# Optimization experiments

Hardware: AMD Instinct MI355X
Metric: run time of the kernel (lower is better)

## Reference

```python
import jax, jax.numpy as jnp
import numpy as np
import math


def _attn(q, k, v):
    # q,k,v: [B, S, d] (d == 1 here). bmm -> scale -> softmax -> bmm.
    scale = 1.0 / math.sqrt(q.shape[2])
    e = jnp.einsum('bsd,btd->bst', q, k) * scale  # [B, S, S]
    w = jax.nn.softmax(e, axis=2)
    return jnp.einsum('bst,btd->bsd', w, v)


def setup_inputs() -> dict:
    key = jax.random.key(0)
    ks = jax.random.split(key, 12)
    B, D = 32, 768
    CLF_OUT = 7
    inp = {}
    names = ['sentence', 'target_spkr_snts', 'other_spkr_snts', 'scene_desc', 'scene_sent']
    for i, name in enumerate(names):
        inp[name] = jax.random.normal(ks[i], (B, D), dtype=jnp.float32)
    inp['W_shared'] = jax.random.normal(ks[5], (768, 512), dtype=jnp.float32) * 0.02
    inp['b_shared'] = jnp.zeros((512,), dtype=jnp.float32)
    inp['W1'] = jax.random.normal(ks[6], (3840, 256), dtype=jnp.float32) * 0.02
    inp['b1'] = jnp.zeros((256,), dtype=jnp.float32)
    inp['W2'] = jax.random.normal(ks[7], (256, CLF_OUT), dtype=jnp.float32) * 0.02
    inp['b2'] = jnp.zeros((CLF_OUT,), dtype=jnp.float32)
    return inp


def reference(sentence, target_spkr_snts, other_spkr_snts, scene_desc, scene_sent,
              W_shared, b_shared, W1, b1, W2, b2):
    B = sentence.shape[0]
    s = sentence[..., None]             # [B, 768, 1]
    sd = scene_desc[..., None]
    ts = target_spkr_snts[..., None]
    oth = other_spkr_snts[..., None]
    ss = scene_sent[..., None]

    speaker_context = _attn(oth, ts, ts)   # [B, 768, 1]
    scene_context = _attn(ss, ss, sd)      # [B, 768, 1]

    sentence_shared = sentence @ W_shared + b_shared                     # [B, 512]
    scene_context_shared = scene_context.reshape(B, -1) @ W_shared + b_shared
    speaker_context_shared = speaker_context.reshape(B, -1) @ W_shared + b_shared

    fused = jnp.concatenate([s, scene_context, speaker_context], axis=1)  # [B, 2304, 1]
    z = _attn(fused, fused, fused)                                        # [B, 2304, 1]

    final = jnp.concatenate([z.reshape(B, -1), sentence_shared,
                             scene_context_shared, speaker_context_shared], axis=1)  # [B, 3840]
    h = jax.nn.relu(final @ W1 + b1)   # dropout is identity in eval mode
    return jax.nn.sigmoid(h @ W2 + b2)  # [B, 7]
```

## Files before the change

### kernel.cpp

```cpp
#include <hip/hip_runtime.h>
#include <math.h>

#define LOG2E 1.44269504088896340736f
typedef float v2f __attribute__((ext_vector_type(2)));


__device__ __forceinline__ void proj_512(
    const float* __restrict__ xsrc,
    const float* __restrict__ Ws,
    const float* __restrict__ bs,
    float* __restrict__ dst,
    float* xb,
    float (*red)[512],
    int tid)
{
    if (tid < 512) { xb[tid] = xsrc[tid]; }
    if (tid >= 256) { xb[tid + 256] = xsrc[tid + 256]; }
    __syncthreads();

    const int g = tid >> 7;
    const int q = tid & 127;
    const float4* __restrict__ Wv = (const float4*)Ws;
    float ax = 0.f, ay = 0.f, az = 0.f, aw = 0.f;
    #pragma unroll 8
    for (int k = g; k < 768; k += 4) {
        const float xv = xb[k];
        const float4 w = Wv[k * 128 + q];
        ax += xv * w.x; ay += xv * w.y; az += xv * w.z; aw += xv * w.w;
    }
    red[g][q * 4 + 0] = ax;
    red[g][q * 4 + 1] = ay;
    red[g][q * 4 + 2] = az;
    red[g][q * 4 + 3] = aw;
    __syncthreads();

    if (tid < 512) {
        float s = bs[tid] + red[0][tid] + red[1][tid] + red[2][tid] + red[3][tid];
        dst[tid] = s;
    }
}

__global__ __launch_bounds__(512) void k1_small_attn_proj0(
    const float* __restrict__ sentence,
    const float* __restrict__ target,
    const float* __restrict__ other,
    const float* __restrict__ scene_desc,
    const float* __restrict__ scene_sent,
    const float* __restrict__ Ws,
    const float* __restrict__ bs,
    float* __restrict__ ctx,
    float* __restrict__ final_)
{
    const int b = blockIdx.x;
    const int y = blockIdx.y;
    const int tid = threadIdx.x;
    __shared__ float s0[768];
    __shared__ float s1[768];
    __shared__ float red[4][512];

    if (y < 24) {
        const int part = y / 12;
        const int rg = y - part * 12;
        const float* qp; const float* kp; const float* vp;
        if (part == 0) { qp = scene_sent + b * 768; kp = qp;               vp = scene_desc + b * 768; }
        else           { qp = other + b * 768;      kp = target + b * 768; vp = kp; }
        for (int i = tid; i < 768; i += 512) { s0[i] = kp[i]; s1[i] = vp[i]; }
        __syncthreads();

        const int r   = rg * 64 + (tid >> 3);
        const int sub = tid & 7;
        const float qL = qp[r] * LOG2E;
        const v2f qL2 = {qL, qL};
        const float4* __restrict__ kv = (const float4*)s0;
        const float4* __restrict__ vv = (const float4*)s1;
        v2f n01 = {0.f, 0.f}, n23 = {0.f, 0.f}, d01 = {0.f, 0.f}, d23 = {0.f, 0.f};
        #pragma unroll 4
        for (int i = 0; i < 24; ++i) {
            const int j = sub + 8 * i;
            const float4 k4 = kv[j];
            const float4 v4 = vv[j];
            const v2f ka = {k4.x, k4.y}, kb = {k4.z, k4.w};
            const v2f va = {v4.x, v4.y}, vbv = {v4.z, v4.w};
            const v2f xa = qL2 * ka, xb2 = qL2 * kb;
            const v2f ea = {__builtin_amdgcn_exp2f(xa.x), __builtin_amdgcn_exp2f(xa.y)};
            const v2f eb = {__builtin_amdgcn_exp2f(xb2.x), __builtin_amdgcn_exp2f(xb2.y)};
            n01 += ea * va;  d01 += ea;
            n23 += eb * vbv; d23 += eb;
        }
        float num = (n01.x + n01.y) + (n23.x + n23.y);
        float den = (d01.x + d01.y) + (d23.x + d23.y);
        num += __shfl_xor(num, 1, 64); num += __shfl_xor(num, 2, 64); num += __shfl_xor(num, 4, 64);
        den += __shfl_xor(den, 1, 64); den += __shfl_xor(den, 2, 64); den += __shfl_xor(den, 4, 64);
        if (sub == 0)
            ctx[b * 1536 + part * 768 + r] = num / den;
    } else {
        proj_512(sentence + b * 768, Ws, bs, final_ + b * 3840 + 2304, s0, red, tid);
    }
}

__global__ __launch_bounds__(512) void k2_fused_attn_proj12(
    const float* __restrict__ sentence,
    const float* __restrict__ ctx,
    const float* __restrict__ Ws,
    const float* __restrict__ bs,
    float* __restrict__ final_)
{
    const int b = blockIdx.x;
    const int y = blockIdx.y;
    const int tid = threadIdx.x;
    __shared__ float vb[2304];
    __shared__ float red[4][512];

    if (y < 36) {
        for (int i = tid; i < 2304; i += 512)
            vb[i] = (i < 768) ? sentence[b * 768 + i] : ctx[b * 1536 + (i - 768)];
        __syncthreads();

        const int r   = y * 64 + (tid >> 3);
        const int sub = tid & 7;
        const float qL = vb[r] * LOG2E;
        const v2f qL2 = {qL, qL};
        const float4* __restrict__ fv = (const float4*)vb;
        v2f n01 = {0.f, 0.f}, n23 = {0.f, 0.f}, d01 = {0.f, 0.f}, d23 = {0.f, 0.f};
        #pragma unroll 4
        for (int i = 0; i < 72; ++i) {
            const int j = sub + 8 * i;
            const float4 f4 = fv[j];
            const v2f fa = {f4.x, f4.y}, fb = {f4.z, f4.w};
            const v2f xa = qL2 * fa, xb2 = qL2 * fb;
            const v2f ea = {__builtin_amdgcn_exp2f(xa.x), __builtin_amdgcn_exp2f(xa.y)};
            const v2f eb = {__builtin_amdgcn_exp2f(xb2.x), __builtin_amdgcn_exp2f(xb2.y)};
            n01 += ea * fa; d01 += ea;
            n23 += eb * fb; d23 += eb;
        }
        float num = (n01.x + n01.y) + (n23.x + n23.y);
        float den = (d01.x + d01.y) + (d23.x + d23.y);
        num += __shfl_xor(num, 1, 64); num += __shfl_xor(num, 2, 64); num += __shfl_xor(num, 4, 64);
        den += __shfl_xor(den, 1, 64); den += __shfl_xor(den, 2, 64); den += __shfl_xor(den, 4, 64);
        if (sub == 0)
            final_[b * 3840 + r] = num / den;
    } else {
        const int p = y - 35;
        proj_512(ctx + b * 1536 + (p - 1) * 768, Ws, bs,
                 final_ + b * 3840 + 2304 + p * 512, vb, red, tid);
    }
}

__global__ __launch_bounds__(1024) void mlp_part_kernel(
    const float* __restrict__ final_,
    const float* __restrict__ W1,
    float* __restrict__ hpart)
{
    const int b = blockIdx.x;
    const int c = blockIdx.y;
    const int tid = threadIdx.x;
    const int base = c * 480;

    __shared__ float fb[480];
    __shared__ float red[16][256];
    if (tid < 480) fb[tid] = final_[b * 3840 + base + tid];
    __syncthreads();

    const int g = tid >> 6;
    const int q = tid & 63;
    const float4* __restrict__ Wv = (const float4*)W1;
    float ax = 0.f, ay = 0.f, az = 0.f, aw = 0.f;
    const int l0 = g * 30;
    #pragma unroll 5
    for (int kk = 0; kk < 30; ++kk) {
        const float xv = fb[l0 + kk];
        const float4 w = Wv[(base + l0 + kk) * 64 + q];
        ax += xv * w.x; ay += xv * w.y; az += xv * w.z; aw += xv * w.w;
    }
    red[g][q * 4 + 0] = ax;
    red[g][q * 4 + 1] = ay;
    red[g][q * 4 + 2] = az;
    red[g][q * 4 + 3] = aw;
    __syncthreads();

    if (tid < 256) {
        float s = 0.f;
        #pragma unroll
        for (int g2 = 0; g2 < 16; ++g2) s += red[g2][tid];
        hpart[(b * 8 + c) * 256 + tid] = s;
    }
}

__global__ __launch_bounds__(512) void mlp_tail_kernel(
    const float* __restrict__ hpart,
    const float* __restrict__ b1,
    const float* __restrict__ W2,
    const float* __restrict__ b2,
    float* __restrict__ out)
{
    const int b = blockIdx.x;
    const int tid = threadIdx.x;

    __shared__ float hb[256];
    if (tid < 256) {
        float s = b1[tid];
        #pragma unroll
        for (int c = 0; c < 8; ++c) s += hpart[(b * 8 + c) * 256 + tid];
        hb[tid] = fmaxf(s, 0.f);
    }
    __syncthreads();

    const int w = tid >> 6;
    const int lane = tid & 63;
    if (w < 7) {
        float a = 0.f;
        #pragma unroll
        for (int c = lane; c < 256; c += 64)
            a += hb[c] * W2[c * 7 + w];
        #pragma unroll
        for (int off = 32; off > 0; off >>= 1)
            a += __shfl_down(a, off, 64);
        if (lane == 0)
            out[b * 7 + w] = 1.f / (1.f + __expf(-(a + b2[w])));
    }
}

extern "C" void kernel_launch(void* const* d_in, const int* in_sizes, int n_in,
                              void* d_out, int out_size, void* d_ws, size_t ws_size,
                              hipStream_t stream) {
    const float* sentence   = (const float*)d_in[0];
    const float* target     = (const float*)d_in[1];
    const float* other      = (const float*)d_in[2];
    const float* scene_desc = (const float*)d_in[3];
    const float* scene_sent = (const float*)d_in[4];
    const float* Ws         = (const float*)d_in[5];
    const float* bs         = (const float*)d_in[6];
    const float* W1         = (const float*)d_in[7];
    const float* b1         = (const float*)d_in[8];
    const float* W2         = (const float*)d_in[9];
    const float* b2         = (const float*)d_in[10];
    float* out = (float*)d_out;

    float* ctx    = (float*)d_ws;
    float* final_ = ctx + 32 * 1536;
    float* hpart  = final_ + 32 * 3840;

    k1_small_attn_proj0<<<dim3(32, 25), 512, 0, stream>>>(sentence, target, other,
                                                          scene_desc, scene_sent,
                                                          Ws, bs, ctx, final_);
    k2_fused_attn_proj12<<<dim3(32, 38), 512, 0, stream>>>(sentence, ctx, Ws, bs, final_);
    mlp_part_kernel<<<dim3(32, 8), 1024, 0, stream>>>(final_, W1, hpart);
    mlp_tail_kernel<<<32, 512, 0, stream>>>(hpart, b1, W2, b2, out);
}
```

Measured before the change: 61.10 us.

## Register-block attention rows per thread and halve block size

The attention loops now give each thread 4 query rows that share every loaded key/value float4, with 16 lanes splitting the key dimension instead of 8. Blocks shrink from 512 to 256 threads, and the projection helper is reworked so each thread handles two k-phases and two output columns. This cuts LDS reads per exp and reduces block-level overhead, but it raises register pressure and lengthens each thread's serial work.

Measured after the change: 66.98 us. +9.6%, slower.

```diff
diff --git a/kernel.cpp b/kernel.cpp
--- a/kernel.cpp
+++ b/kernel.cpp
@@ -5,17 +5,16 @@
 typedef float v2f __attribute__((ext_vector_type(2)));
 
 
-__device__ __forceinline__ void proj_512(
+__device__ __forceinline__ void proj_256(
     const float* __restrict__ xsrc,
     const float* __restrict__ Ws,
     const float* __restrict__ bs,
     float* __restrict__ dst,
     float* xb,
-    float (*red)[512],
+    float* redf,
     int tid)
 {
-    if (tid < 512) { xb[tid] = xsrc[tid]; }
-    if (tid >= 256) { xb[tid + 256] = xsrc[tid + 256]; }
+    for (int i = tid; i < 768; i += 256) xb[i] = xsrc[i];
     __syncthreads();
 
     const int g = tid >> 7;
@@ -23,24 +22,70 @@
     const float4* __restrict__ Wv = (const float4*)Ws;
     float ax = 0.f, ay = 0.f, az = 0.f, aw = 0.f;
     #pragma unroll 8
-    for (int k = g; k < 768; k += 4) {
+    for (int k = g; k < 768; k += 2) {
         const float xv = xb[k];
         const float4 w = Wv[k * 128 + q];
         ax += xv * w.x; ay += xv * w.y; az += xv * w.z; aw += xv * w.w;
     }
-    red[g][q * 4 + 0] = ax;
-    red[g][q * 4 + 1] = ay;
-    red[g][q * 4 + 2] = az;
-    red[g][q * 4 + 3] = aw;
-    __syncthreads();
-
-    if (tid < 512) {
-        float s = bs[tid] + red[0][tid] + red[1][tid] + red[2][tid] + red[3][tid];
-        dst[tid] = s;
-    }
-}
-
-__global__ __launch_bounds__(512) void k1_small_attn_proj0(
+    redf[g * 512 + q * 4 + 0] = ax;
+    redf[g * 512 + q * 4 + 1] = ay;
+    redf[g * 512 + q * 4 + 2] = az;
+    redf[g * 512 + q * 4 + 3] = aw;
+    __syncthreads();
+
+    dst[tid]       = bs[tid]       + redf[tid]       + redf[512 + tid];
+    dst[tid + 256] = bs[tid + 256] + redf[tid + 256] + redf[512 + tid + 256];
+}
+
+__device__ __forceinline__ void attn_r4(
+    const float* __restrict__ qsrc,
+    const float4* __restrict__ kv,
+    const float4* __restrict__ vv,
+    int n4, int rbase, int tid,
+    float* __restrict__ outp)
+{
+    const int i0  = rbase + (tid >> 4);
+    const int sub = tid & 15;
+    v2f q2[4];
+    #pragma unroll
+    for (int m = 0; m < 4; ++m) {
+        const float qL = qsrc[i0 + 16 * m] * LOG2E;
+        q2[m] = (v2f){qL, qL};
+    }
+    v2f n0[4], n1[4], d0[4], d1[4];
+    #pragma unroll
+    for (int m = 0; m < 4; ++m) {
+        n0[m] = (v2f){0.f, 0.f}; n1[m] = (v2f){0.f, 0.f};
+        d0[m] = (v2f){0.f, 0.f}; d1[m] = (v2f){0.f, 0.f};
+    }
+    #pragma unroll 2
+    for (int j = sub; j < n4; j += 16) {
+        const float4 k4 = kv[j];
+        const float4 v4 = vv[j];
+        const v2f ka = {k4.x, k4.y}, kb = {k4.z, k4.w};
+        const v2f va = {v4.x, v4.y}, vb2 = {v4.z, v4.w};
+        #pragma unroll
+        for (int m = 0; m < 4; ++m) {
+            const v2f xa = q2[m] * ka, xb = q2[m] * kb;
+            const v2f ea = {__builtin_amdgcn_exp2f(xa.x), __builtin_amdgcn_exp2f(xa.y)};
+            const v2f eb = {__builtin_amdgcn_exp2f(xb.x), __builtin_amdgcn_exp2f(xb.y)};
+            n0[m] += ea * va;  d0[m] += ea;
+            n1[m] += eb * vb2; d1[m] += eb;
+        }
+    }
+    #pragma unroll
+    for (int m = 0; m < 4; ++m) {
+        float num = (n0[m].x + n0[m].y) + (n1[m].x + n1[m].y);
+        float den = (d0[m].x + d0[m].y) + (d1[m].x + d1[m].y);
+        num += __shfl_xor(num, 1, 64); num += __shfl_xor(num, 2, 64);
+        num += __shfl_xor(num, 4, 64); num += __shfl_xor(num, 8, 64);
+        den += __shfl_xor(den, 1, 64); den += __shfl_xor(den, 2, 64);
+        den += __shfl_xor(den, 4, 64); den += __shfl_xor(den, 8, 64);
+        if (sub == 0) outp[i0 + 16 * m] = num / den;
+    }
+}
+
+__global__ __launch_bounds__(256) void k1_small_attn_proj0(
     const float* __restrict__ sentence,
     const float* __restrict__ target,
     const float* __restrict__ other,
@@ -56,7 +101,7 @@
     const int tid = threadIdx.x;
     __shared__ float s0[768];
     __shared__ float s1[768];
-    __shared__ float red[4][512];
+    __shared__ float redf[1024];
 
     if (y < 24) {
         const int part = y / 12;
@@ -64,41 +109,16 @@
         const float* qp; const float* kp; const float* vp;
         if (part == 0) { qp = scene_sent + b * 768; kp = qp;               vp = scene_desc + b * 768; }
         else           { qp = other + b * 768;      kp = target + b * 768; vp = kp; }
-        for (int i = tid; i < 768; i += 512) { s0[i] = kp[i]; s1[i] = vp[i]; }
+        for (int i = tid; i < 768; i += 256) { s0[i] = kp[i]; s1[i] = vp[i]; }
         __syncthreads();
-
-        const int r   = rg * 64 + (tid >> 3);
-        const int sub = tid & 7;
-        const float qL = qp[r] * LOG2E;
-        const v2f qL2 = {qL, qL};
-        const float4* __restrict__ kv = (const float4*)s0;
-        const float4* __restrict__ vv = (const float4*)s1;
-        v2f n01 = {0.f, 0.f}, n23 = {0.f, 0.f}, d01 = {0.f, 0.f}, d23 = {0.f, 0.f};
-        #pragma unroll 4
-        for (int i = 0; i < 24; ++i) {
-            const int j = sub + 8 * i;
-            const float4 k4 = kv[j];
-            const float4 v4 = vv[j];
-            const v2f ka = {k4.x, k4.y}, kb = {k4.z, k4.w};
-            const v2f va = {v4.x, v4.y}, vbv = {v4.z, v4.w};
-            const v2f xa = qL2 * ka, xb2 = qL2 * kb;
-            const v2f ea = {__builtin_amdgcn_exp2f(xa.x), __builtin_amdgcn_exp2f(xa.y)};
-            const v2f eb = {__builtin_amdgcn_exp2f(xb2.x), __builtin_amdgcn_exp2f(xb2.y)};
-            n01 += ea * va;  d01 += ea;
-            n23 += eb * vbv; d23 += eb;
-        }
-        float num = (n01.x + n01.y) + (n23.x + n23.y);
-        float den = (d01.x + d01.y) + (d23.x + d23.y);
-        num += __shfl_xor(num, 1, 64); num += __shfl_xor(num, 2, 64); num += __shfl_xor(num, 4, 64);
-        den += __shfl_xor(den, 1, 64); den += __shfl_xor(den, 2, 64); den += __shfl_xor(den, 4, 64);
-        if (sub == 0)
-            ctx[b * 1536 + part * 768 + r] = num / den;
+        attn_r4(qp, (const float4*)s0, (const float4*)s1, 192,
+                rg * 64, tid, ctx + b * 1536 + part * 768);
     } else {
-        proj_512(sentence + b * 768, Ws, bs, final_ + b * 3840 + 2304, s0, red, tid);
-    }
-}
-
-__global__ __launch_bounds__(512) void k2_fused_attn_proj12(
+        proj_256(sentence + b * 768, Ws, bs, final_ + b * 3840 + 2304, s0, redf, tid);
+    }
+}
+
+__global__ __launch_bounds__(256) void k2_fused_attn_proj12(
     const float* __restrict__ sentence,
     const float* __restrict__ ctx,
     const float* __restrict__ Ws,
@@ -109,40 +129,18 @@
     const int y = blockIdx.y;
     const int tid = threadIdx.x;
     __shared__ float vb[2304];
-    __shared__ float red[4][512];
+    __shared__ float redf[1024];
 
     if (y < 36) {
-        for (int i = tid; i < 2304; i += 512)
+        for (int i = tid; i < 2304; i += 256)
             vb[i] = (i < 768) ? sentence[b * 768 + i] : ctx[b * 1536 + (i - 768)];
         __syncthreads();
-
-        const int r   = y * 64 + (tid >> 3);
-        const int sub = tid & 7;
-        const float qL = vb[r] * LOG2E;
-        const v2f qL2 = {qL, qL};
-        const float4* __restrict__ fv = (const float4*)vb;
-        v2f n01 = {0.f, 0.f}, n23 = {0.f, 0.f}, d01 = {0.f, 0.f}, d23 = {0.f, 0.f};
-        #pragma unroll 4
-        for (int i = 0; i < 72; ++i) {
-            const int j = sub + 8 * i;
-            const float4 f4 = fv[j];
-            const v2f fa = {f4.x, f4.y}, fb = {f4.z, f4.w};
-            const v2f xa = qL2 * fa, xb2 = qL2 * fb;
-            const v2f ea = {__builtin_amdgcn_exp2f(xa.x), __builtin_amdgcn_exp2f(xa.y)};
-            const v2f eb = {__builtin_amdgcn_exp2f(xb2.x), __builtin_amdgcn_exp2f(xb2.y)};
-            n01 += ea * fa; d01 += ea;
-            n23 += eb * fb; d23 += eb;
-        }
-        float num = (n01.x + n01.y) + (n23.x + n23.y);
-        float den = (d01.x + d01.y) + (d23.x + d23.y);
-        num += __shfl_xor(num, 1, 64); num += __shfl_xor(num, 2, 64); num += __shfl_xor(num, 4, 64);
-        den += __shfl_xor(den, 1, 64); den += __shfl_xor(den, 2, 64); den += __shfl_xor(den, 4, 64);
-        if (sub == 0)
-            final_[b * 3840 + r] = num / den;
+        attn_r4(vb, (const float4*)vb, (const float4*)vb, 576,
+                y * 64, tid, final_ + b * 3840);
     } else {
         const int p = y - 35;
-        proj_512(ctx + b * 1536 + (p - 1) * 768, Ws, bs,
-                 final_ + b * 3840 + 2304 + p * 512, vb, red, tid);
+        proj_256(ctx + b * 1536 + (p - 1) * 768, Ws, bs,
+                 final_ + b * 3840 + 2304 + p * 512, vb, redf, tid);
     }
 }
 
@@ -240,10 +238,10 @@
     float* final_ = ctx + 32 * 1536;
     float* hpart  = final_ + 32 * 3840;
 
-    k1_small_attn_proj0<<<dim3(32, 25), 512, 0, stream>>>(sentence, target, other,
+    k1_small_attn_proj0<<<dim3(32, 25), 256, 0, stream>>>(sentence, target, other,
                                                           scene_desc, scene_sent,
                                                           Ws, bs, ctx, final_);
-    k2_fused_attn_proj12<<<dim3(32, 38), 512, 0, stream>>>(sentence, ctx, Ws, bs, final_);
+    k2_fused_attn_proj12<<<dim3(32, 38), 256, 0, stream>>>(sentence, ctx, Ws, bs, final_);
     mlp_part_kernel<<<dim3(32, 8), 1024, 0, stream>>>(final_, W1, hpart);
     mlp_tail_kernel<<<32, 512, 0, stream>>>(hpart, b1, W2, b2, out);
 }
```
